# Kernel tuning notes

Hardware: AMD Instinct MI355X
Metric: run time of the kernel (lower is better)

## Reference

```python
import jax, jax.numpy as jnp
import numpy as np

BZ, QL, KL, D = 8, 2048, 2048, 128
SCALE = 1.0 / (D ** 0.5)
NEG = -1000000000.0


def setup_inputs() -> dict:
    key = jax.random.key(0)
    kq, kk, kv, km = jax.random.split(key, 4)
    q = jax.random.normal(kq, (BZ, QL, D), dtype=jnp.float32)
    k = jax.random.normal(kk, (BZ, KL, D), dtype=jnp.float32)
    v = jax.random.normal(kv, (BZ, KL, D), dtype=jnp.float32)
    mask = jax.random.randint(km, (BZ, KL), 0, 2).astype(jnp.bool_)
    return {"q": q, "k": k, "v": v, "mask": mask}


def reference(q, k, v, mask):
    # scores: (bz, q_len, k_len)
    score = jnp.einsum('bqd,bkd->bqk', q, k) * SCALE
    # masked_fill where ~mask (padding positions) with -1e9
    score = jnp.where(mask[:, None, :], score, NEG)
    weights = jax.nn.softmax(score, axis=-1)
    # (bz, q_len, v_dim)
    return jnp.einsum('bqk,bkd->bqd', weights, v)
```

## Files before the change

kernel.cpp:

```cpp
#include <hip/hip_runtime.h>
#include <hip/hip_bf16.h>


#define BZ 8
#define QL 2048
#define KLEN 2048
#define DH 128
#define NSL 64
#define SLICE_E 4096
#define PPITCH 40

typedef float f32x4 __attribute__((ext_vector_type(4)));
typedef int   i32x4 __attribute__((ext_vector_type(4)));
typedef __bf16 bf16x8 __attribute__((ext_vector_type(8)));
typedef __bf16 bf16x4 __attribute__((ext_vector_type(4)));
typedef __bf16 bf16x2 __attribute__((ext_vector_type(2)));

#define QSC 0.12751879523298232f
#define NEGV -1000000000.0f

__global__ void prep_kv(const float* __restrict__ kg, const float* __restrict__ vg,
                        __bf16* __restrict__ khat, __bf16* __restrict__ vhat) {
  const int blk = blockIdx.x;
  const int bs = blk & 511;
  const int b = bs >> 6, s = bs & 63;
  const int tid = threadIdx.x;
#pragma unroll
  for (int i = 0; i < 2; ++i) {
    const int c = i * 256 + tid;
    const int ln = c & 63, lc = ln & 15, qd = ln >> 4;
    if (blk < 512) {
      const int ff = (c >> 6) & 1, kf = c >> 7;
      const int key = s * 32 + ff * 16 + lc;
      const float* src = kg + ((size_t)(b * KLEN + key)) * DH + kf * 32 + qd * 8;
      f32x4 a = *(const f32x4*)src;
      f32x4 d = *(const f32x4*)(src + 4);
      bf16x8 w;
      w[0]=(__bf16)a[0]; w[1]=(__bf16)a[1]; w[2]=(__bf16)a[2]; w[3]=(__bf16)a[3];
      w[4]=(__bf16)d[0]; w[5]=(__bf16)d[1]; w[6]=(__bf16)d[2]; w[7]=(__bf16)d[3];
      *(bf16x8*)&khat[((size_t)bs * 512 + c) * 8] = w;
    } else {
      const int nt = c >> 6;
      const float* src = vg + ((size_t)(b * KLEN + s * 32 + qd * 8)) * DH + nt * 16 + lc;
      bf16x8 w;
#pragma unroll
      for (int j = 0; j < 8; ++j) w[j] = (__bf16)src[(size_t)j * DH];
      *(bf16x8*)&vhat[((size_t)bs * 512 + c) * 8] = w;
    }
  }
}

__global__ __launch_bounds__(512, 2) void fattn7(
    const __bf16* __restrict__ khat, const __bf16* __restrict__ vhat,
    const float* __restrict__ qg_, const int* __restrict__ maskg,
    float* __restrict__ outg) {
  __shared__ __align__(16) __bf16 sP[8][2][16 * PPITCH];
  __shared__ __align__(16) float fb[8192 + 64];

  const int tid = threadIdx.x;
  const int wv = tid >> 6, ln = tid & 63;
  const int qd = ln >> 4, lc = ln & 15;
  const int ab = blockIdx.x & 7, qt = blockIdx.x >> 3;
  const int q0 = qt * 64;
  const int qg = wv & 1, sl = wv >> 1;

  bf16x8 qf[2][4];
#pragma unroll
  for (int qp = 0; qp < 2; ++qp) {
    const float* qr = qg_ + ((size_t)(ab * QL + q0 + qg * 32 + qp * 16 + lc)) * DH + qd * 8;
#pragma unroll
    for (int kf = 0; kf < 4; ++kf) {
      f32x4 a = *(const f32x4*)(qr + kf * 32);
      f32x4 c = *(const f32x4*)(qr + kf * 32 + 4);
      bf16x8 t;
      t[0]=(__bf16)(a[0]*QSC); t[1]=(__bf16)(a[1]*QSC); t[2]=(__bf16)(a[2]*QSC); t[3]=(__bf16)(a[3]*QSC);
      t[4]=(__bf16)(c[0]*QSC); t[5]=(__bf16)(c[1]*QSC); t[6]=(__bf16)(c[2]*QSC); t[7]=(__bf16)(c[3]*QSC);
      qf[qp][kf] = t;
    }
  }

  const __bf16* Kb = khat + (size_t)ab * NSL * SLICE_E;
  const __bf16* Vb = vhat + (size_t)ab * NSL * SLICE_E;
  const int* mrow = maskg + ab * KLEN;
  __bf16* sp0 = &sP[wv][0][0];
  __bf16* sp1 = &sP[wv][1][0];

  f32x4 oacc[2][8];
#pragma unroll
  for (int qp = 0; qp < 2; ++qp)
#pragma unroll
    for (int i = 0; i < 8; ++i) oacc[qp][i] = (f32x4){0.f, 0.f, 0.f, 0.f};
  float li[2] = {0.f, 0.f};

  bf16x8 kA[4][2], kN[4][2], vA[8];
  {
    const __bf16* ks = Kb + (size_t)(sl * 16) * SLICE_E;
#pragma unroll
    for (int kf = 0; kf < 4; ++kf)
#pragma unroll
      for (int f = 0; f < 2; ++f)
        kA[kf][f] = *(const bf16x8*)&ks[((kf * 2 + f) * 64 + ln) * 8];
  }
  i32x4 mc0 = *(const i32x4*)&mrow[sl * 16 * 32 + qd * 4];
  i32x4 mc1 = *(const i32x4*)&mrow[sl * 16 * 32 + 16 + qd * 4];

  for (int it = 0; it < 16; ++it) {
    const int s = sl * 16 + it;
    const __bf16* vs = Vb + (size_t)s * SLICE_E;

#pragma unroll
    for (int nt = 0; nt < 8; ++nt)
      vA[nt] = *(const bf16x8*)&vs[(nt * 64 + ln) * 8];

    const int sn = (it < 15) ? s + 1 : s;
    const __bf16* ksn = Kb + (size_t)sn * SLICE_E;
#pragma unroll
    for (int kf = 0; kf < 4; ++kf)
#pragma unroll
      for (int f = 0; f < 2; ++f)
        kN[kf][f] = *(const bf16x8*)&ksn[((kf * 2 + f) * 64 + ln) * 8];
    i32x4 mn0 = *(const i32x4*)&mrow[sn * 32 + qd * 4];
    i32x4 mn1 = *(const i32x4*)&mrow[sn * 32 + 16 + qd * 4];

    f32x4 sa[2][2];
#pragma unroll
    for (int f = 0; f < 2; ++f)
#pragma unroll
      for (int qp = 0; qp < 2; ++qp) sa[f][qp] = (f32x4){0.f, 0.f, 0.f, 0.f};
#pragma unroll
    for (int kf = 0; kf < 4; ++kf)
#pragma unroll
      for (int f = 0; f < 2; ++f) {
        sa[f][0] = __builtin_amdgcn_mfma_f32_16x16x32_bf16(kA[kf][f], qf[0][kf], sa[f][0], 0, 0, 0);
        sa[f][1] = __builtin_amdgcn_mfma_f32_16x16x32_bf16(kA[kf][f], qf[1][kf], sa[f][1], 0, 0, 0);
      }

#pragma unroll
    for (int qp = 0; qp < 2; ++qp) {
      float ps[2][4];
#pragma unroll
      for (int r = 0; r < 4; ++r) {
        float p0 = __builtin_amdgcn_exp2f(sa[0][qp][r]);
        float p1 = __builtin_amdgcn_exp2f(sa[1][qp][r]);
        ps[0][r] = mc0[r] ? p0 : 0.f;
        ps[1][r] = mc1[r] ? p1 : 0.f;
      }
      li[qp] += ((ps[0][0] + ps[0][1]) + (ps[0][2] + ps[0][3])) +
                ((ps[1][0] + ps[1][1]) + (ps[1][2] + ps[1][3]));
      __bf16* sp = (qp == 0) ? sp0 : sp1;
#pragma unroll
      for (int f = 0; f < 2; ++f) {
        bf16x4 pw;
        pw[0] = (__bf16)ps[f][0]; pw[1] = (__bf16)ps[f][1];
        pw[2] = (__bf16)ps[f][2]; pw[3] = (__bf16)ps[f][3];
        *(bf16x4*)&sp[lc * PPITCH + f * 16 + qd * 4] = pw;
      }
    }
    bf16x8 pf0 = *(const bf16x8*)&sp0[lc * PPITCH + qd * 8];
    bf16x8 pf1 = *(const bf16x8*)&sp1[lc * PPITCH + qd * 8];

#pragma unroll
    for (int nt = 0; nt < 8; ++nt) {
      oacc[0][nt] = __builtin_amdgcn_mfma_f32_16x16x32_bf16(vA[nt], pf0, oacc[0][nt], 0, 0, 0);
      oacc[1][nt] = __builtin_amdgcn_mfma_f32_16x16x32_bf16(vA[nt], pf1, oacc[1][nt], 0, 0, 0);
    }

#pragma unroll
    for (int kf = 0; kf < 4; ++kf)
#pragma unroll
      for (int f = 0; f < 2; ++f) kA[kf][f] = kN[kf][f];
    mc0 = mn0; mc1 = mn1;
  }

#pragma unroll
  for (int qp = 0; qp < 2; ++qp) {
    li[qp] += __shfl_xor(li[qp], 16, 64);
    li[qp] += __shfl_xor(li[qp], 32, 64);
  }

  f32x4* mOv = (f32x4*)fb;
  float* sml = fb + 8192;
  auto publish = [&]() {
#pragma unroll
    for (int qp = 0; qp < 2; ++qp) {
#pragma unroll
      for (int nt = 0; nt < 8; ++nt)
        mOv[((qg * 2 + qp) * 8 + nt) * 64 + ln] = oacc[qp][nt];
      if (qd == 0) sml[(qg * 2 + qp) * 16 + lc] = li[qp];
    }
  };
  auto absorb = [&]() {
#pragma unroll
    for (int qp = 0; qp < 2; ++qp) {
      li[qp] += sml[(qg * 2 + qp) * 16 + lc];
#pragma unroll
      for (int nt = 0; nt < 8; ++nt) {
        f32x4 o2 = mOv[((qg * 2 + qp) * 8 + nt) * 64 + ln];
#pragma unroll
        for (int r = 0; r < 4; ++r) oacc[qp][nt][r] += o2[r];
      }
    }
  };

  __syncthreads();
  if (sl == 3) publish();
  __syncthreads();
  if (sl == 2) absorb();
  __syncthreads();
  if (sl == 1) publish();
  __syncthreads();
  if (sl == 0) absorb();
  __syncthreads();
  if (sl == 2) publish();
  __syncthreads();
  if (sl == 0) {
    absorb();
#pragma unroll
    for (int qp = 0; qp < 2; ++qp) {
      const float invL = 1.0f / li[qp];
      float* orow = outg + ((size_t)(ab * QL + q0 + qg * 32 + qp * 16 + lc)) * DH;
#pragma unroll
      for (int nt = 0; nt < 8; ++nt) {
        f32x4 res;
#pragma unroll
        for (int r = 0; r < 4; ++r) res[r] = oacc[qp][nt][r] * invL;
        *(f32x4*)&orow[nt * 16 + qd * 4] = res;
      }
    }
  }
}

#define KT 64
#define KPITCH 136
#define VPITCH 72
#define PPITCH2 72

__global__ __launch_bounds__(256, 1) void fattn_mono(
    const float* __restrict__ qgp, const float* __restrict__ kg,
    const float* __restrict__ vg, const int* __restrict__ maskg,
    float* __restrict__ outg) {
  __shared__ __bf16 sK[KT][KPITCH];
  __shared__ __bf16 sVT[DH][VPITCH];
  __shared__ __bf16 sPm[4][16][PPITCH2];

  const int tid = threadIdx.x;
  const int wv = tid >> 6, ln = tid & 63;
  const int qd = ln >> 4, lc = ln & 15;
  const int bid = blockIdx.x;
  const int b = bid >> 5;
  const int q0 = (bid & 31) << 6;
  const int qw = q0 + (wv << 4);

  bf16x8 qf[4];
  {
    const float* qr = qgp + ((size_t)(b * QL + qw + lc)) * DH + qd * 8;
#pragma unroll
    for (int kf = 0; kf < 4; ++kf) {
      f32x4 a = *(const f32x4*)(qr + kf * 32);
      f32x4 c = *(const f32x4*)(qr + kf * 32 + 4);
      bf16x8 t;
      t[0]=(__bf16)(a[0]*QSC); t[1]=(__bf16)(a[1]*QSC); t[2]=(__bf16)(a[2]*QSC); t[3]=(__bf16)(a[3]*QSC);
      t[4]=(__bf16)(c[0]*QSC); t[5]=(__bf16)(c[1]*QSC); t[6]=(__bf16)(c[2]*QSC); t[7]=(__bf16)(c[3]*QSC);
      qf[kf] = t;
    }
  }

  const float* kb = kg + (size_t)b * KLEN * DH;
  const float* vb = vg + (size_t)b * KLEN * DH;
  const int* mrow = maskg + b * KLEN;

  f32x4 kreg[8], va[4], vbr[4];

  auto load_tile = [&](int t) {
    const float* kt = kb + ((size_t)t * KT) * DH;
#pragma unroll
    for (int it = 0; it < 8; ++it) {
      int f = it * 256 + tid;
      kreg[it] = *(const f32x4*)(kt + (size_t)(f >> 5) * DH + (f & 31) * 4);
    }
    const float* vt = vb + ((size_t)t * KT) * DH;
#pragma unroll
    for (int it = 0; it < 4; ++it) {
      int u = it * 256 + tid;
      int m = u & 31, dc = (u >> 5) * 4;
      va[it]  = *(const f32x4*)(vt + (size_t)(2 * m) * DH + dc);
      vbr[it] = *(const f32x4*)(vt + (size_t)(2 * m + 1) * DH + dc);
    }
  };
  auto store_tile = [&]() {
#pragma unroll
    for (int it = 0; it < 8; ++it) {
      int f = it * 256 + tid;
      bf16x4 w;
      w[0]=(__bf16)kreg[it][0]; w[1]=(__bf16)kreg[it][1];
      w[2]=(__bf16)kreg[it][2]; w[3]=(__bf16)kreg[it][3];
      *(bf16x4*)&sK[f >> 5][(f & 31) * 4] = w;
    }
#pragma unroll
    for (int it = 0; it < 4; ++it) {
      int u = it * 256 + tid;
      int m = u & 31, dc = (u >> 5) * 4;
#pragma unroll
      for (int j = 0; j < 4; ++j) {
        bf16x2 p2;
        p2[0] = (__bf16)va[it][j];
        p2[1] = (__bf16)vbr[it][j];
        *(bf16x2*)&sVT[dc + j][2 * m] = p2;
      }
    }
  };

  f32x4 oacc[8];
#pragma unroll
  for (int i = 0; i < 8; ++i) oacc[i] = (f32x4){0.f, 0.f, 0.f, 0.f};
  float mi[4] = {-INFINITY, -INFINITY, -INFINITY, -INFINITY};
  float li[4] = {0.f, 0.f, 0.f, 0.f};

  load_tile(0); store_tile(); __syncthreads();

  for (int t = 0; t < (KLEN / KT); ++t) {
    const bool more = (t + 1 < (KLEN / KT));
    if (more) load_tile(t + 1);

    f32x4 sa[4];
#pragma unroll
    for (int f = 0; f < 4; ++f) sa[f] = (f32x4){0.f, 0.f, 0.f, 0.f};
#pragma unroll
    for (int kf = 0; kf < 4; ++kf)
#pragma unroll
      for (int f = 0; f < 4; ++f) {
        bf16x8 bk = *(const bf16x8*)&sK[f * 16 + lc][kf * 32 + qd * 8];
        sa[f] = __builtin_amdgcn_mfma_f32_16x16x32_bf16(qf[kf], bk, sa[f], 0, 0, 0);
      }

    const int kv0 = t * KT;
#pragma unroll
    for (int f = 0; f < 4; ++f) {
      const bool keep = mrow[kv0 + f * 16 + lc] != 0;
#pragma unroll
      for (int r = 0; r < 4; ++r) sa[f][r] = keep ? sa[f][r] : NEGV;
    }

    float rm[4], alpha[4], rs[4];
#pragma unroll
    for (int r = 0; r < 4; ++r)
      rm[r] = fmaxf(fmaxf(sa[0][r], sa[1][r]), fmaxf(sa[2][r], sa[3][r]));
#pragma unroll
    for (int sh = 0; sh < 4; ++sh) {
      const int off = 1 << sh;
#pragma unroll
      for (int r = 0; r < 4; ++r) rm[r] = fmaxf(rm[r], __shfl_xor(rm[r], off, 64));
    }
#pragma unroll
    for (int r = 0; r < 4; ++r) {
      float mn = fmaxf(mi[r], rm[r]);
      alpha[r] = __builtin_amdgcn_exp2f(mi[r] - mn);
      mi[r] = mn; rs[r] = 0.f;
    }
#pragma unroll
    for (int f = 0; f < 4; ++f)
#pragma unroll
      for (int r = 0; r < 4; ++r) {
        float p = __builtin_amdgcn_exp2f(sa[f][r] - mi[r]);
        sa[f][r] = p; rs[r] += p;
      }
#pragma unroll
    for (int sh = 0; sh < 4; ++sh) {
      const int off = 1 << sh;
#pragma unroll
      for (int r = 0; r < 4; ++r) rs[r] += __shfl_xor(rs[r], off, 64);
    }
#pragma unroll
    for (int r = 0; r < 4; ++r) li[r] = li[r] * alpha[r] + rs[r];

#pragma unroll
    for (int f = 0; f < 4; ++f)
#pragma unroll
      for (int r = 0; r < 4; ++r)
        sPm[wv][qd * 4 + r][f * 16 + lc] = (__bf16)sa[f][r];
#pragma unroll
    for (int nt = 0; nt < 8; ++nt)
#pragma unroll
      for (int r = 0; r < 4; ++r) oacc[nt][r] *= alpha[r];

#pragma unroll
    for (int kp = 0; kp < 2; ++kp) {
      bf16x8 ap = *(const bf16x8*)&sPm[wv][lc][kp * 32 + qd * 8];
#pragma unroll
      for (int nt = 0; nt < 8; ++nt) {
        bf16x8 bv = *(const bf16x8*)&sVT[nt * 16 + lc][kp * 32 + qd * 8];
        oacc[nt] = __builtin_amdgcn_mfma_f32_16x16x32_bf16(ap, bv, oacc[nt], 0, 0, 0);
      }
    }

    __syncthreads();
    if (more) store_tile();
    __syncthreads();
  }

  float inv[4];
#pragma unroll
  for (int r = 0; r < 4; ++r) inv[r] = 1.0f / li[r];
  float* orow = outg + ((size_t)(b * QL + qw)) * DH;
#pragma unroll
  for (int nt = 0; nt < 8; ++nt)
#pragma unroll
    for (int r = 0; r < 4; ++r)
      orow[(size_t)(qd * 4 + r) * DH + nt * 16 + lc] = oacc[nt][r] * inv[r];
}

extern "C" void kernel_launch(void* const* d_in, const int* in_sizes, int n_in,
                              void* d_out, int out_size, void* d_ws, size_t ws_size,
                              hipStream_t stream) {
  (void)in_sizes; (void)n_in; (void)out_size;
  const float* q = (const float*)d_in[0];
  const float* k = (const float*)d_in[1];
  const float* v = (const float*)d_in[2];
  const int* mask = (const int*)d_in[3];
  float* out = (float*)d_out;

  const size_t kv_elems = (size_t)BZ * KLEN * DH;
  if (ws_size >= 2 * kv_elems * sizeof(__bf16)) {
    __bf16* khat = (__bf16*)d_ws;
    __bf16* vhat = khat + kv_elems;
    prep_kv<<<dim3(1024), dim3(256), 0, stream>>>(k, v, khat, vhat);
    fattn7<<<dim3(256), dim3(512), 0, stream>>>(khat, vhat, q, mask, out);
  } else {
    fattn_mono<<<dim3(BZ * (QL / 64)), dim3(256), 0, stream>>>(q, k, v, mask, out);
  }
}
```

Measured before the change: 118.4 us.

## Halve per-block query tile and split keys across eight waves

Each block now handles 32 queries instead of 64. All eight waves process the same queries, each over its own eighth of the key slices, so the grid doubles to 512 blocks. Partial outputs are merged with a longer LDS publish/absorb tree. The intent is better CU coverage and latency hiding through more blocks and waves in flight. The cost is doubled K/V reads per query, more barriers in the reduction, and a tighter register budget from launch_bounds(512,4), which risks spills.

```diff
diff --git a/kernel.cpp b/kernel.cpp
--- a/kernel.cpp
+++ b/kernel.cpp
@@ -50,7 +50,7 @@
   }
 }
 
-__global__ __launch_bounds__(512, 2) void fattn7(
+__global__ __launch_bounds__(512, 4) void fattn8(
     const __bf16* __restrict__ khat, const __bf16* __restrict__ vhat,
     const float* __restrict__ qg_, const int* __restrict__ maskg,
     float* __restrict__ outg) {
@@ -61,13 +61,13 @@
   const int wv = tid >> 6, ln = tid & 63;
   const int qd = ln >> 4, lc = ln & 15;
   const int ab = blockIdx.x & 7, qt = blockIdx.x >> 3;
-  const int q0 = qt * 64;
-  const int qg = wv & 1, sl = wv >> 1;
+  const int q0 = qt * 32;
+  const int sl = wv;
 
   bf16x8 qf[2][4];
 #pragma unroll
   for (int qp = 0; qp < 2; ++qp) {
-    const float* qr = qg_ + ((size_t)(ab * QL + q0 + qg * 32 + qp * 16 + lc)) * DH + qd * 8;
+    const float* qr = qg_ + ((size_t)(ab * QL + q0 + qp * 16 + lc)) * DH + qd * 8;
 #pragma unroll
     for (int kf = 0; kf < 4; ++kf) {
       f32x4 a = *(const f32x4*)(qr + kf * 32);
@@ -94,25 +94,25 @@
 
   bf16x8 kA[4][2], kN[4][2], vA[8];
   {
-    const __bf16* ks = Kb + (size_t)(sl * 16) * SLICE_E;
+    const __bf16* ks = Kb + (size_t)(sl * 8) * SLICE_E;
 #pragma unroll
     for (int kf = 0; kf < 4; ++kf)
 #pragma unroll
       for (int f = 0; f < 2; ++f)
         kA[kf][f] = *(const bf16x8*)&ks[((kf * 2 + f) * 64 + ln) * 8];
   }
-  i32x4 mc0 = *(const i32x4*)&mrow[sl * 16 * 32 + qd * 4];
-  i32x4 mc1 = *(const i32x4*)&mrow[sl * 16 * 32 + 16 + qd * 4];
-
-  for (int it = 0; it < 16; ++it) {
-    const int s = sl * 16 + it;
+  i32x4 mc0 = *(const i32x4*)&mrow[sl * 8 * 32 + qd * 4];
+  i32x4 mc1 = *(const i32x4*)&mrow[sl * 8 * 32 + 16 + qd * 4];
+
+  for (int it = 0; it < 8; ++it) {
+    const int s = sl * 8 + it;
     const __bf16* vs = Vb + (size_t)s * SLICE_E;
 
 #pragma unroll
     for (int nt = 0; nt < 8; ++nt)
       vA[nt] = *(const bf16x8*)&vs[(nt * 64 + ln) * 8];
 
-    const int sn = (it < 15) ? s + 1 : s;
+    const int sn = (it < 7) ? s + 1 : s;
     const __bf16* ksn = Kb + (size_t)sn * SLICE_E;
 #pragma unroll
     for (int kf = 0; kf < 4; ++kf)
@@ -180,22 +180,22 @@
 
   f32x4* mOv = (f32x4*)fb;
   float* sml = fb + 8192;
-  auto publish = [&]() {
+  auto publish = [&](int slot) {
 #pragma unroll
     for (int qp = 0; qp < 2; ++qp) {
 #pragma unroll
       for (int nt = 0; nt < 8; ++nt)
-        mOv[((qg * 2 + qp) * 8 + nt) * 64 + ln] = oacc[qp][nt];
-      if (qd == 0) sml[(qg * 2 + qp) * 16 + lc] = li[qp];
+        mOv[((slot * 2 + qp) * 8 + nt) * 64 + ln] = oacc[qp][nt];
+      if (qd == 0) sml[(slot * 2 + qp) * 16 + lc] = li[qp];
     }
   };
-  auto absorb = [&]() {
+  auto absorb = [&](int slot) {
 #pragma unroll
     for (int qp = 0; qp < 2; ++qp) {
-      li[qp] += sml[(qg * 2 + qp) * 16 + lc];
+      li[qp] += sml[(slot * 2 + qp) * 16 + lc];
 #pragma unroll
       for (int nt = 0; nt < 8; ++nt) {
-        f32x4 o2 = mOv[((qg * 2 + qp) * 8 + nt) * 64 + ln];
+        f32x4 o2 = mOv[((slot * 2 + qp) * 8 + nt) * 64 + ln];
 #pragma unroll
         for (int r = 0; r < 4; ++r) oacc[qp][nt][r] += o2[r];
       }
@@ -203,22 +203,32 @@
   };
 
   __syncthreads();
-  if (sl == 3) publish();
-  __syncthreads();
-  if (sl == 2) absorb();
-  __syncthreads();
-  if (sl == 1) publish();
-  __syncthreads();
-  if (sl == 0) absorb();
-  __syncthreads();
-  if (sl == 2) publish();
-  __syncthreads();
-  if (sl == 0) {
-    absorb();
+  if (wv == 5) publish(0);
+  if (wv == 7) publish(1);
+  __syncthreads();
+  if (wv == 4) absorb(0);
+  if (wv == 6) absorb(1);
+  __syncthreads();
+  if (wv == 4) publish(0);
+  if (wv == 6) publish(1);
+  __syncthreads();
+  if (wv == 0) absorb(0);
+  if (wv == 2) absorb(1);
+  __syncthreads();
+  if (wv == 1) publish(0);
+  if (wv == 3) publish(1);
+  __syncthreads();
+  if (wv == 0) absorb(0);
+  if (wv == 2) absorb(1);
+  __syncthreads();
+  if (wv == 2) publish(0);
+  __syncthreads();
+  if (wv == 0) {
+    absorb(0);
 #pragma unroll
     for (int qp = 0; qp < 2; ++qp) {
       const float invL = 1.0f / li[qp];
-      float* orow = outg + ((size_t)(ab * QL + q0 + qg * 32 + qp * 16 + lc)) * DH;
+      float* orow = outg + ((size_t)(ab * QL + q0 + qp * 16 + lc)) * DH;
 #pragma unroll
       for (int nt = 0; nt < 8; ++nt) {
         f32x4 res;
@@ -424,7 +434,7 @@
     __bf16* khat = (__bf16*)d_ws;
     __bf16* vhat = khat + kv_elems;
     prep_kv<<<dim3(1024), dim3(256), 0, stream>>>(k, v, khat, vhat);
-    fattn7<<<dim3(256), dim3(512), 0, stream>>>(khat, vhat, q, mask, out);
+    fattn8<<<dim3(512), dim3(512), 0, stream>>>(khat, vhat, q, mask, out);
   } else {
     fattn_mono<<<dim3(BZ * (QL / 64)), dim3(256), 0, stream>>>(q, k, v, mask, out);
   }
```

Result: slower. 162.4 us (+37.2%).
